# Optimization experiments

Measured on AMD Instinct MI355X. Metric: run time of the kernel, lower is better.

The kernel has to match this reference:

```python
import jax, jax.numpy as jnp
import numpy as np

N = 100000        # nodes
E = 1600000       # edges (avg degree 16)
F_IN = 128        # num_node_features
H = 64            # hidden_channels
F_EDGE = 8        # num_edge_features (output dim per edge)


def setup_inputs() -> dict:
    key = jax.random.key(0)
    ks = jax.random.split(key, 9)
    x = jax.random.normal(ks[0], (N, F_IN), dtype=jnp.float32)
    edge_index = jax.random.randint(ks[1], (2, E), 0, N, dtype=jnp.int32)
    s = 0.05
    W1 = jax.random.normal(ks[2], (F_IN, H), jnp.float32) * s
    b1 = jnp.zeros((H,), jnp.float32)
    W2 = jax.random.normal(ks[3], (H, H), jnp.float32) * s
    b2 = jnp.zeros((H,), jnp.float32)
    Wl = jax.random.normal(ks[4], (2 * H, F_EDGE), jnp.float32) * s
    bl = jnp.zeros((F_EDGE,), jnp.float32)
    return {"x": x, "edge_index": edge_index,
            "W1": W1, "b1": b1, "W2": W2, "b2": b2, "Wl": Wl, "bl": bl}


def gcn_conv(x, W, b, row, col, n):
    # GCNConv: h = D^{-1/2} (A + I) D^{-1/2} (x W) + b
    h = x @ W
    sl = jnp.arange(n, dtype=row.dtype)          # self-loops
    r = jnp.concatenate([row, sl])
    c = jnp.concatenate([col, sl])
    ones = jnp.ones(r.shape[0], dtype=h.dtype)
    deg = jax.ops.segment_sum(ones, c, num_segments=n)      # in-degree incl. self-loop
    dinv = jax.lax.rsqrt(jnp.maximum(deg, 1e-12))
    norm = dinv[r] * dinv[c]                                 # symmetric normalization
    agg = jax.ops.segment_sum(norm[:, None] * h[r], c, num_segments=n)
    return agg + b


def reference(x, edge_index, W1, b1, W2, b2, Wl, bl):
    row, col = edge_index[0], edge_index[1]
    h = jax.nn.relu(gcn_conv(x, W1, b1, row, col, N))
    # dropout p=0.5 is identity at inference (training=False)
    h = jax.nn.relu(gcn_conv(h, W2, b2, row, col, N))
    x_i = h[row]                                  # [E, H]
    x_j = h[col]                                  # [E, H]
    return jnp.concatenate([x_i, x_j], axis=-1) @ Wl + bl   # [E, F_EDGE]
```

## Files before the change

kernel.cpp:

```cpp
#include <hip/hip_runtime.h>
#include <hip/hip_bf16.h>

static constexpr int NN  = 100000;
static constexpr int NE  = 1600000;
static constexpr int FIN = 128;
static constexpr int HD  = 64;

static constexpr int NB    = 256;
static constexpr int NPB   = 392;
static constexpr int EPB   = NE / NB;
static constexpr unsigned long long DIV392_MAGIC = 43826197ULL;

typedef __attribute__((ext_vector_type(8))) short bf16x8;
typedef __attribute__((ext_vector_type(4))) float f32x4;

__device__ __forceinline__ float bf2f(unsigned short u) {
    return __uint_as_float(((unsigned int)u) << 16);
}
__device__ __forceinline__ unsigned short f2bf(float f) {
    __hip_bfloat16 hb = __float2bfloat16(f);
    return *(unsigned short*)&hb;
}
__device__ __forceinline__ int bucket_of(int c) {
    return (int)(((unsigned long long)(unsigned int)c * DIV392_MAGIC) >> 34);
}

__device__ __forceinline__ float load_in(const void* p, size_t i, int isbf) {
    return isbf ? bf2f(((const unsigned short*)p)[i]) : ((const float*)p)[i];
}

__global__ __launch_bounds__(256) void k_hist(const int* __restrict__ col, int* __restrict__ hist,
                                              const unsigned short* __restrict__ xu,
                                              int* __restrict__ flag) {
    __shared__ int h[4][NB];
    int t = threadIdx.x, w = t >> 6;
#pragma unroll
    for (int r = 0; r < 4; ++r) h[r][t] = 0;
    __syncthreads();
    int base = blockIdx.x * EPB;
    for (int e = base + t; e < base + EPB; e += 256)
        atomicAdd(&h[w][bucket_of(col[e])], 1);
    __syncthreads();
    hist[t * NB + blockIdx.x] = h[0][t] + h[1][t] + h[2][t] + h[3][t];
    if (blockIdx.x == 0) {
        __syncthreads();
        int cnt = 0;
        for (int k = t; k < 4096; k += 256) {
            unsigned short u = xu[2 * k];
            int ex = (u >> 7) & 0xFF;
            cnt += (ex >= 110 && ex <= 135) ? 1 : 0;
        }
        h[0][t] = cnt;
        __syncthreads();
        for (int off = 128; off > 0; off >>= 1) {
            if (t < off) h[0][t] += h[0][t + off];
            __syncthreads();
        }
        if (t == 0) flag[0] = (h[0][0] >= 2048) ? 1 : 0;
    }
}

__global__ __launch_bounds__(256) void k_gscan1(int* __restrict__ a, int* __restrict__ bsums) {
    __shared__ int sd[256];
    int t = threadIdx.x;
    int base = blockIdx.x * 1024 + t * 4;
    int v0 = a[base], v1 = a[base + 1], v2 = a[base + 2], v3 = a[base + 3];
    int tsum = v0 + v1 + v2 + v3;
    sd[t] = tsum;
    __syncthreads();
    for (int off = 1; off < 256; off <<= 1) {
        int tmp = (t >= off) ? sd[t - off] : 0;
        __syncthreads();
        sd[t] += tmp;
        __syncthreads();
    }
    int run = sd[t] - tsum;
    a[base] = run; run += v0;
    a[base + 1] = run; run += v1;
    a[base + 2] = run; run += v2;
    a[base + 3] = run;
    if (t == 255) bsums[blockIdx.x] = sd[t];
}

__device__ __forceinline__ void scan_bsums(const int* __restrict__ bsumsRaw, int* sb) {
    int t = threadIdx.x;
    int myv = 0;
    if (t < 64) { myv = bsumsRaw[t]; sb[t] = myv; }
    __syncthreads();
    for (int off = 1; off < 64; off <<= 1) {
        int v = (t < 64 && t >= off) ? sb[t - off] : 0;
        __syncthreads();
        if (t < 64) sb[t] += v;
        __syncthreads();
    }
    if (t < 64) sb[t] -= myv;
    __syncthreads();
}

__global__ __launch_bounds__(256) void k_binfill(const int* __restrict__ row, const int* __restrict__ col,
                                                 const int* __restrict__ histS,
                                                 const int* __restrict__ bsumsRaw,
                                                 int* __restrict__ csr_tmp) {
    __shared__ int cur[NB];
    __shared__ int sb[64];
    int t = threadIdx.x;
    scan_bsums(bsumsRaw, sb);
    cur[t] = histS[t * NB + blockIdx.x] + sb[t >> 2];
    __syncthreads();
    int base = blockIdx.x * EPB;
    for (int e = base + t; e < base + EPB; e += 256) {
        int r = row[e], c = col[e];
        int b = bucket_of(c);
        int p = atomicAdd(&cur[b], 1);
        csr_tmp[p] = r | ((c - b * NPB) << 17);
    }
}

__global__ __launch_bounds__(256) void k_bsort(const int* __restrict__ csr_tmp,
                                               const int* __restrict__ histS,
                                               const int* __restrict__ bsumsRaw,
                                               int* __restrict__ csr_src,
                                               int* __restrict__ start,
                                               float* __restrict__ dinv) {
    __shared__ int cnt[512];
    __shared__ int cur[512];
    __shared__ int sb[64];
    int t = threadIdx.x;
    int k = blockIdx.x;
    cnt[t] = 0; cnt[t + 256] = 0;
    scan_bsums(bsumsRaw, sb);
    int S = histS[k * NB] + sb[k >> 2];
    int E = (k < NB - 1) ? (histS[(k + 1) * NB] + sb[(k + 1) >> 2]) : NE;
    int nbase = k * NPB;
    __syncthreads();
    for (int e = S + t; e < E; e += 256)
        atomicAdd(&cnt[csr_tmp[e] >> 17], 1);
    __syncthreads();
    int rc0 = cnt[t], rc1 = cnt[t + 256];
    for (int d = 1; d < 512; d <<= 1) {
        int idx = (t + 1) * (d << 1) - 1;
        if (idx < 512) cnt[idx] += cnt[idx - d];
        __syncthreads();
    }
    if (t == 0) cnt[511] = 0;
    __syncthreads();
    for (int d = 256; d >= 1; d >>= 1) {
        int idx = (t + 1) * (d << 1) - 1;
        if (idx < 512) { int tmp = cnt[idx - d]; cnt[idx - d] = cnt[idx]; cnt[idx] += tmp; }
        __syncthreads();
    }
    int n0 = nbase + t;
    if (n0 < NN) {
        start[n0] = S + cnt[t] + rc0;
        dinv[n0] = rsqrtf((float)(rc0 + 1));
    }
    int li = t + 256;
    int n1 = nbase + li;
    if (li < NPB && n1 < NN) {
        start[n1] = S + cnt[li] + rc1;
        dinv[n1] = rsqrtf((float)(rc1 + 1));
    }
    cur[t] = cnt[t]; cur[t + 256] = cnt[t + 256];
    __syncthreads();
    for (int e = S + t; e < E; e += 256) {
        int u = csr_tmp[e];
        int p = atomicAdd(&cur[u >> 17], 1);
        csr_src[S + p] = u & 0x1FFFF;
    }
}

template <int K, bool XDUAL>
__global__ __launch_bounds__(256) void k_gemm_mfma(const void* __restrict__ X,
                                                   const void* __restrict__ W,
                                                   const float* __restrict__ dinv,
                                                   unsigned short* __restrict__ T,
                                                   const int* __restrict__ flag) {
    constexpr int KT = K / 32;
    __shared__ unsigned short Bs[KT * 4 * 64 * 8];
    int isbf = flag[0];
    for (int tup = threadIdx.x; tup < KT * 4 * 64; tup += 256) {
        int l  = tup & 63;
        int nt = (tup >> 6) & 3;
        int kt = tup >> 8;
        int n  = nt * 16 + (l & 15);
        int kb = kt * 32 + (l >> 4) * 8;
        unsigned short tmp[8];
#pragma unroll
        for (int j = 0; j < 8; ++j) tmp[j] = f2bf(load_in(W, (size_t)(kb + j) * HD + n, isbf));
        *((uint4*)&Bs[(size_t)tup * 8]) = *((const uint4*)tmp);
    }
    __syncthreads();
    int wave = threadIdx.x >> 6, lane = threadIdx.x & 63;
    int quad = lane >> 4, m = lane & 15;
    int row0 = blockIdx.x * 64 + wave * 16;
    int row  = row0 + m;
    int rowc = (row < NN) ? row : (NN - 1);
    bool xf32 = XDUAL && (isbf == 0);
    const char* xrow = (const char*)X + (size_t)rowc * K * (xf32 ? 4 : 2);
    f32x4 acc[4];
#pragma unroll
    for (int nt = 0; nt < 4; ++nt) acc[nt] = (f32x4){0.f, 0.f, 0.f, 0.f};
#pragma unroll
    for (int kt = 0; kt < KT; ++kt) {
        bf16x8 a;
        if (!xf32) {
            a = *((const bf16x8*)(xrow + (size_t)(kt * 32 + quad * 8) * 2));
        } else {
            const float4* fp = (const float4*)(xrow + (size_t)(kt * 32 + quad * 8) * 4);
            float4 u0 = fp[0], u1 = fp[1];
            unsigned short tmp[8] = {f2bf(u0.x), f2bf(u0.y), f2bf(u0.z), f2bf(u0.w),
                                     f2bf(u1.x), f2bf(u1.y), f2bf(u1.z), f2bf(u1.w)};
            a = *((const bf16x8*)tmp);
        }
#pragma unroll
        for (int nt = 0; nt < 4; ++nt) {
            bf16x8 b = *((const bf16x8*)&Bs[(size_t)((kt * 4 + nt) * 64 + lane) * 8]);
            acc[nt] = __builtin_amdgcn_mfma_f32_16x16x32_bf16(a, b, acc[nt], 0, 0, 0);
        }
    }
#pragma unroll
    for (int r = 0; r < 4; ++r) {
        int orow = row0 + quad * 4 + r;
        if (orow < NN) {
            float sc = dinv[orow];
#pragma unroll
            for (int nt = 0; nt < 4; ++nt)
                T[(size_t)orow * 64 + nt * 16 + m] = f2bf(acc[nt][r] * sc);
        }
    }
}

__device__ __forceinline__ void agg_to_lds(const unsigned short* __restrict__ T,
                                           const int* __restrict__ endOff,
                                           const int* __restrict__ csr_src,
                                           const float* __restrict__ dinv,
                                           const void* __restrict__ bias, int isbf,
                                           unsigned short (*hS)[72], int i0) {
    int lane = threadIdx.x & 63, wave = threadIdx.x >> 6;
    int g  = lane >> 3;
    int fl = (lane & 7) * 8;
    int li = wave * 8 + g;
    int i  = i0 + li;
    int end = endOff[i];
    int beg = (i == 0) ? 0 : endOff[i - 1];
    union U { uint4 u; unsigned short s[8]; };
    float a[8];
    {
        U t; t.u = *((const uint4*)(T + (size_t)i * 64 + fl));
#pragma unroll
        for (int j = 0; j < 8; ++j) a[j] = bf2f(t.s[j]);
    }
    int k = beg;
    for (; k + 3 < end; k += 4) {
        int s0 = csr_src[k], s1 = csr_src[k + 1], s2 = csr_src[k + 2], s3 = csr_src[k + 3];
        U t0, t1, t2, t3;
        t0.u = *((const uint4*)(T + (size_t)s0 * 64 + fl));
        t1.u = *((const uint4*)(T + (size_t)s1 * 64 + fl));
        t2.u = *((const uint4*)(T + (size_t)s2 * 64 + fl));
        t3.u = *((const uint4*)(T + (size_t)s3 * 64 + fl));
#pragma unroll
        for (int j = 0; j < 8; ++j)
            a[j] += bf2f(t0.s[j]) + bf2f(t1.s[j]) + bf2f(t2.s[j]) + bf2f(t3.s[j]);
    }
    for (; k < end; ++k) {
        int s = csr_src[k];
        U t; t.u = *((const uint4*)(T + (size_t)s * 64 + fl));
#pragma unroll
        for (int j = 0; j < 8; ++j) a[j] += bf2f(t.s[j]);
    }
    float di = dinv[i];
    U o;
#pragma unroll
    for (int j = 0; j < 8; ++j)
        o.s[j] = f2bf(fmaxf(fmaf(di, a[j], load_in(bias, fl + j, isbf)), 0.f));
    *((uint4*)&hS[li][fl]) = o.u;
}

__global__ __launch_bounds__(256) void k_agg_gemm(const unsigned short* __restrict__ T,
                                                  const int* __restrict__ endOff,
                                                  const int* __restrict__ csr_src,
                                                  const float* __restrict__ dinv,
                                                  const void* __restrict__ bias,
                                                  const void* __restrict__ W2,
                                                  const int* __restrict__ flag,
                                                  unsigned short* __restrict__ Tb) {
    __shared__ unsigned short hS[32][72];
    __shared__ unsigned short Bs[2 * 4 * 64 * 8];
    int isbf = flag[0];
    for (int tup = threadIdx.x; tup < 512; tup += 256) {
        int l  = tup & 63;
        int nt = (tup >> 6) & 3;
        int kt = tup >> 8;
        int n  = nt * 16 + (l & 15);
        int kb = kt * 32 + (l >> 4) * 8;
        unsigned short tmp[8];
#pragma unroll
        for (int j = 0; j < 8; ++j) tmp[j] = f2bf(load_in(W2, (size_t)(kb + j) * HD + n, isbf));
        *((uint4*)&Bs[(size_t)tup * 8]) = *((const uint4*)tmp);
    }
    int i0 = blockIdx.x * 32;
    agg_to_lds(T, endOff, csr_src, dinv, bias, isbf, hS, i0);
    __syncthreads();
    int wave = threadIdx.x >> 6, lane = threadIdx.x & 63;
    int quad = lane >> 4, m = lane & 15;
    int tile = wave >> 1;
    int nb   = (wave & 1) * 2;
    f32x4 acc0 = (f32x4){0.f, 0.f, 0.f, 0.f};
    f32x4 acc1 = (f32x4){0.f, 0.f, 0.f, 0.f};
#pragma unroll
    for (int kt = 0; kt < 2; ++kt) {
        bf16x8 a  = *((const bf16x8*)&hS[tile * 16 + m][kt * 32 + quad * 8]);
        bf16x8 b0 = *((const bf16x8*)&Bs[(size_t)((kt * 4 + nb) * 64 + lane) * 8]);
        bf16x8 b1 = *((const bf16x8*)&Bs[(size_t)((kt * 4 + nb + 1) * 64 + lane) * 8]);
        acc0 = __builtin_amdgcn_mfma_f32_16x16x32_bf16(a, b0, acc0, 0, 0, 0);
        acc1 = __builtin_amdgcn_mfma_f32_16x16x32_bf16(a, b1, acc1, 0, 0, 0);
    }
#pragma unroll
    for (int r = 0; r < 4; ++r) {
        int orow = i0 + tile * 16 + quad * 4 + r;
        float sc = dinv[orow];
        Tb[(size_t)orow * 64 + nb * 16 + m]       = f2bf(acc0[r] * sc);
        Tb[(size_t)orow * 64 + (nb + 1) * 16 + m] = f2bf(acc1[r] * sc);
    }
}

__global__ __launch_bounds__(256) void k_agg_pgemm(const unsigned short* __restrict__ T,
                                                   const int* __restrict__ endOff,
                                                   const int* __restrict__ csr_src,
                                                   const float* __restrict__ dinv,
                                                   const void* __restrict__ bias,
                                                   const void* __restrict__ Wl,
                                                   const void* __restrict__ bl,
                                                   const int* __restrict__ flag,
                                                   unsigned short* __restrict__ P) {
    __shared__ unsigned short hS[32][72];
    int isbf = flag[0];
    int lane = threadIdx.x & 63;
    int quad = lane >> 4, m = lane & 15;
    bf16x8 bfr[2];
#pragma unroll
    for (int kt = 0; kt < 2; ++kt) {
        unsigned short tmp[8];
#pragma unroll
        for (int j = 0; j < 8; ++j) {
            int kk = kt * 32 + quad * 8 + j;
            float w = (m < 8) ? load_in(Wl, (size_t)kk * 8 + m, isbf)
                              : load_in(Wl, (size_t)(64 + kk) * 8 + (m - 8), isbf);
            tmp[j] = f2bf(w);
        }
        bfr[kt] = *((const bf16x8*)tmp);
    }
    float binit = (m < 8) ? load_in(bl, m, isbf) : 0.f;
    int i0 = blockIdx.x * 32;
    agg_to_lds(T, endOff, csr_src, dinv, bias, isbf, hS, i0);
    __syncthreads();
    int wave = threadIdx.x >> 6;
    if (wave < 2) {
        f32x4 acc = (f32x4){binit, binit, binit, binit};
#pragma unroll
        for (int kt = 0; kt < 2; ++kt) {
            bf16x8 a = *((const bf16x8*)&hS[wave * 16 + m][kt * 32 + quad * 8]);
            acc = __builtin_amdgcn_mfma_f32_16x16x32_bf16(a, bfr[kt], acc, 0, 0, 0);
        }
#pragma unroll
        for (int r = 0; r < 4; ++r) {
            int orow = i0 + wave * 16 + quad * 4 + r;
            P[(size_t)orow * 16 + m] = f2bf(acc[r]);
        }
    }
}

__global__ __launch_bounds__(256) void k_edge_add(const unsigned short* __restrict__ P,
                                                  const int* __restrict__ erow,
                                                  const int* __restrict__ ecol,
                                                  void* __restrict__ out,
                                                  const int* __restrict__ flag) {
    int isbf = flag[0];
    int e = blockIdx.x * 256 + threadIdx.x;
    int i = erow[e], j = ecol[e];
    ushort4 r0 = *((const ushort4*)(P + (size_t)i * 16));
    ushort4 r1 = *((const ushort4*)(P + (size_t)i * 16 + 4));
    ushort4 c0 = *((const ushort4*)(P + (size_t)j * 16 + 8));
    ushort4 c1 = *((const ushort4*)(P + (size_t)j * 16 + 12));
    float v[8] = {bf2f(r0.x) + bf2f(c0.x), bf2f(r0.y) + bf2f(c0.y),
                  bf2f(r0.z) + bf2f(c0.z), bf2f(r0.w) + bf2f(c0.w),
                  bf2f(r1.x) + bf2f(c1.x), bf2f(r1.y) + bf2f(c1.y),
                  bf2f(r1.z) + bf2f(c1.z), bf2f(r1.w) + bf2f(c1.w)};
    if (isbf) {
        union { unsigned short h[8]; uint4 u; } p;
#pragma unroll
        for (int o = 0; o < 8; ++o) p.h[o] = f2bf(v[o]);
        *((uint4*)((__hip_bfloat16*)out + (size_t)e * 8)) = p.u;
    } else {
        float* op = (float*)out + (size_t)e * 8;
        ((float4*)op)[0] = make_float4(v[0], v[1], v[2], v[3]);
        ((float4*)op)[1] = make_float4(v[4], v[5], v[6], v[7]);
    }
}

extern "C" void kernel_launch(void* const* d_in, const int* in_sizes, int n_in,
                              void* d_out, int out_size, void* d_ws, size_t ws_size,
                              hipStream_t stream) {
    const void* x  = d_in[0];
    const int*  ei = (const int*)d_in[1];
    const void* W1 = d_in[2];
    const void* b1 = d_in[3];
    const void* W2 = d_in[4];
    const void* b2 = d_in[5];
    const void* Wl = d_in[6];
    const void* bl = d_in[7];
    const int* row = ei;
    const int* col = ei + NE;

    char* ws = (char*)d_ws;
    int*   flag    = (int*)ws;    ws += 16;
    int*   hist    = (int*)ws;    ws += (size_t)NB * NB * 4;
    int*   bsums   = (int*)ws;    ws += 256 * 4;
    int*   start   = (int*)ws;    ws += (size_t)NN * 4;
    float* dinv    = (float*)ws;  ws += (size_t)NN * 4;
    int*   csr_tmp = (int*)ws;    ws += (size_t)NE * 4;
    int*   csr_src = (int*)ws;    ws += (size_t)NE * 4;
    unsigned short* T  = (unsigned short*)ws;  ws += (size_t)NN * 64 * 2;
    unsigned short* Tb = (unsigned short*)ws;  ws += (size_t)NN * 64 * 2;
    unsigned short* P  = (unsigned short*)ws;

    int gE   = (NE + 255) / 256;
    int gN32 = NN / 32;
    int gN64 = (NN + 63) / 64;

    k_hist   <<<NB, 256, 0, stream>>>(col, hist, (const unsigned short*)x, flag);
    k_gscan1 <<<64, 256, 0, stream>>>(hist, bsums);
    k_binfill<<<NB, 256, 0, stream>>>(row, col, hist, bsums, csr_tmp);
    k_bsort  <<<NB, 256, 0, stream>>>(csr_tmp, hist, bsums, csr_src, start, dinv);

    k_gemm_mfma<FIN, true><<<gN64, 256, 0, stream>>>(x, W1, dinv, T, flag);

    k_agg_gemm <<<gN32, 256, 0, stream>>>(T, start, csr_src, dinv, b1, W2, flag, Tb);

    k_agg_pgemm<<<gN32, 256, 0, stream>>>(Tb, start, csr_src, dinv, b2, Wl, bl, flag, P);

    k_edge_add <<<gE, 256, 0, stream>>>(P, row, col, d_out, flag);
}
```

Before: 293.0 us.

## Split node features into 16-column slices and unfuse aggregation from GEMMs

Feature matrices are stored as four 16-column slices, each NN x 16 contiguous, so each aggregation block gathers from one 3.2MB slice that can stay cache-resident. Aggregation moves to a standalone kernel that splits each node's neighbour list across four lanes, combines their partial sums with shuffles, and adds the self term afterwards. The dense GEMMs become separate kernels that read the sliced layout. The cost is extra launches and a round trip through global memory for H4, in exchange for better cache locality and more parallelism in the gather.

```diff
diff --git a/kernel.cpp b/kernel.cpp
--- a/kernel.cpp
+++ b/kernel.cpp
@@ -10,6 +10,8 @@
 static constexpr int NPB   = 392;
 static constexpr int EPB   = NE / NB;
 static constexpr unsigned long long DIV392_MAGIC = 43826197ULL;
+
+static constexpr int NSL = 4;
 
 typedef __attribute__((ext_vector_type(8))) short bf16x8;
 typedef __attribute__((ext_vector_type(4))) float f32x4;
@@ -173,7 +175,7 @@
 __global__ __launch_bounds__(256) void k_gemm_mfma(const void* __restrict__ X,
                                                    const void* __restrict__ W,
                                                    const float* __restrict__ dinv,
-                                                   unsigned short* __restrict__ T,
+                                                   unsigned short* __restrict__ T4,
                                                    const int* __restrict__ flag) {
     constexpr int KT = K / 32;
     __shared__ unsigned short Bs[KT * 4 * 64 * 8];
@@ -225,66 +227,74 @@
             float sc = dinv[orow];
 #pragma unroll
             for (int nt = 0; nt < 4; ++nt)
-                T[(size_t)orow * 64 + nt * 16 + m] = f2bf(acc[nt][r] * sc);
-        }
-    }
-}
-
-__device__ __forceinline__ void agg_to_lds(const unsigned short* __restrict__ T,
-                                           const int* __restrict__ endOff,
-                                           const int* __restrict__ csr_src,
-                                           const float* __restrict__ dinv,
-                                           const void* __restrict__ bias, int isbf,
-                                           unsigned short (*hS)[72], int i0) {
-    int lane = threadIdx.x & 63, wave = threadIdx.x >> 6;
-    int g  = lane >> 3;
-    int fl = (lane & 7) * 8;
-    int li = wave * 8 + g;
-    int i  = i0 + li;
+                T4[((size_t)nt * NN + orow) * 16 + m] = f2bf(acc[nt][r] * sc);
+        }
+    }
+}
+
+__global__ __launch_bounds__(256) void k_agg4(const unsigned short* __restrict__ T4,
+                                              const int* __restrict__ endOff,
+                                              const int* __restrict__ csr_src,
+                                              const float* __restrict__ dinv,
+                                              const void* __restrict__ bias,
+                                              const int* __restrict__ flag,
+                                              unsigned short* __restrict__ H4) {
+    int isbf = flag[0];
+    int slice = blockIdx.x & 3;
+    int grp   = blockIdx.x >> 2;
+    int t = threadIdx.x;
+    int li   = t >> 3;
+    int slot = (t >> 1) & 3;
+    int fl   = (t & 1) * 8;
+    int i = grp * 32 + li;
     int end = endOff[i];
     int beg = (i == 0) ? 0 : endOff[i - 1];
+    const unsigned short* Ts = T4 + (size_t)slice * NN * 16;
     union U { uint4 u; unsigned short s[8]; };
     float a[8];
-    {
-        U t; t.u = *((const uint4*)(T + (size_t)i * 64 + fl));
-#pragma unroll
-        for (int j = 0; j < 8; ++j) a[j] = bf2f(t.s[j]);
-    }
-    int k = beg;
-    for (; k + 3 < end; k += 4) {
-        int s0 = csr_src[k], s1 = csr_src[k + 1], s2 = csr_src[k + 2], s3 = csr_src[k + 3];
-        U t0, t1, t2, t3;
-        t0.u = *((const uint4*)(T + (size_t)s0 * 64 + fl));
-        t1.u = *((const uint4*)(T + (size_t)s1 * 64 + fl));
-        t2.u = *((const uint4*)(T + (size_t)s2 * 64 + fl));
-        t3.u = *((const uint4*)(T + (size_t)s3 * 64 + fl));
-#pragma unroll
-        for (int j = 0; j < 8; ++j)
-            a[j] += bf2f(t0.s[j]) + bf2f(t1.s[j]) + bf2f(t2.s[j]) + bf2f(t3.s[j]);
-    }
-    for (; k < end; ++k) {
-        int s = csr_src[k];
-        U t; t.u = *((const uint4*)(T + (size_t)s * 64 + fl));
-#pragma unroll
-        for (int j = 0; j < 8; ++j) a[j] += bf2f(t.s[j]);
-    }
+#pragma unroll
+    for (int j = 0; j < 8; ++j) a[j] = 0.f;
+    int k = beg + slot;
+    int sA = (k < end) ? csr_src[k] : -1;
+    int sB = (k + 4 < end) ? csr_src[k + 4] : -1;
+    while (sA >= 0) {
+        U rA, rB;
+        rA.u = *((const uint4*)(Ts + (size_t)sA * 16 + fl));
+        bool hb = (sB >= 0);
+        if (hb) rB.u = *((const uint4*)(Ts + (size_t)sB * 16 + fl));
+        k += 8;
+        sA = (k < end) ? csr_src[k] : -1;
+        sB = (k + 4 < end) ? csr_src[k + 4] : -1;
+#pragma unroll
+        for (int j = 0; j < 8; ++j) a[j] += bf2f(rA.s[j]);
+        if (hb) {
+#pragma unroll
+            for (int j = 0; j < 8; ++j) a[j] += bf2f(rB.s[j]);
+        }
+    }
+#pragma unroll
+    for (int j = 0; j < 8; ++j) {
+        a[j] += __shfl_xor(a[j], 2, 64);
+        a[j] += __shfl_xor(a[j], 4, 64);
+    }
+    U sf; sf.u = *((const uint4*)(Ts + (size_t)i * 16 + fl));
     float di = dinv[i];
     U o;
 #pragma unroll
-    for (int j = 0; j < 8; ++j)
-        o.s[j] = f2bf(fmaxf(fmaf(di, a[j], load_in(bias, fl + j, isbf)), 0.f));
-    *((uint4*)&hS[li][fl]) = o.u;
-}
-
-__global__ __launch_bounds__(256) void k_agg_gemm(const unsigned short* __restrict__ T,
-                                                  const int* __restrict__ endOff,
-                                                  const int* __restrict__ csr_src,
-                                                  const float* __restrict__ dinv,
-                                                  const void* __restrict__ bias,
-                                                  const void* __restrict__ W2,
-                                                  const int* __restrict__ flag,
-                                                  unsigned short* __restrict__ Tb) {
-    __shared__ unsigned short hS[32][72];
+    for (int j = 0; j < 8; ++j) {
+        float v = a[j] + bf2f(sf.s[j]);
+        float b = load_in(bias, (size_t)(slice * 16 + fl + j), isbf);
+        o.s[j] = f2bf(fmaxf(fmaf(di, v, b), 0.f));
+    }
+    if (slot == 0)
+        *((uint4*)(H4 + ((size_t)slice * NN + i) * 16 + fl)) = o.u;
+}
+
+__global__ __launch_bounds__(256) void k_gemm_h(const unsigned short* __restrict__ H4,
+                                                const void* __restrict__ W,
+                                                const float* __restrict__ dinv,
+                                                unsigned short* __restrict__ Tb4,
+                                                const int* __restrict__ flag) {
     __shared__ unsigned short Bs[2 * 4 * 64 * 8];
     int isbf = flag[0];
     for (int tup = threadIdx.x; tup < 512; tup += 256) {
@@ -295,47 +305,47 @@
         int kb = kt * 32 + (l >> 4) * 8;
         unsigned short tmp[8];
 #pragma unroll
-        for (int j = 0; j < 8; ++j) tmp[j] = f2bf(load_in(W2, (size_t)(kb + j) * HD + n, isbf));
+        for (int j = 0; j < 8; ++j) tmp[j] = f2bf(load_in(W, (size_t)(kb + j) * HD + n, isbf));
         *((uint4*)&Bs[(size_t)tup * 8]) = *((const uint4*)tmp);
     }
-    int i0 = blockIdx.x * 32;
-    agg_to_lds(T, endOff, csr_src, dinv, bias, isbf, hS, i0);
     __syncthreads();
     int wave = threadIdx.x >> 6, lane = threadIdx.x & 63;
     int quad = lane >> 4, m = lane & 15;
-    int tile = wave >> 1;
-    int nb   = (wave & 1) * 2;
-    f32x4 acc0 = (f32x4){0.f, 0.f, 0.f, 0.f};
-    f32x4 acc1 = (f32x4){0.f, 0.f, 0.f, 0.f};
+    int row0 = blockIdx.x * 64 + wave * 16;
+    int row  = row0 + m;
+    int rowc = (row < NN) ? row : (NN - 1);
+    f32x4 acc[4];
+#pragma unroll
+    for (int nt = 0; nt < 4; ++nt) acc[nt] = (f32x4){0.f, 0.f, 0.f, 0.f};
 #pragma unroll
     for (int kt = 0; kt < 2; ++kt) {
-        bf16x8 a  = *((const bf16x8*)&hS[tile * 16 + m][kt * 32 + quad * 8]);
-        bf16x8 b0 = *((const bf16x8*)&Bs[(size_t)((kt * 4 + nb) * 64 + lane) * 8]);
-        bf16x8 b1 = *((const bf16x8*)&Bs[(size_t)((kt * 4 + nb + 1) * 64 + lane) * 8]);
-        acc0 = __builtin_amdgcn_mfma_f32_16x16x32_bf16(a, b0, acc0, 0, 0, 0);
-        acc1 = __builtin_amdgcn_mfma_f32_16x16x32_bf16(a, b1, acc1, 0, 0, 0);
+        int k0 = kt * 32 + quad * 8;
+        bf16x8 a = *((const bf16x8*)&H4[((size_t)(k0 >> 4) * NN + rowc) * 16 + (k0 & 15)]);
+#pragma unroll
+        for (int nt = 0; nt < 4; ++nt) {
+            bf16x8 b = *((const bf16x8*)&Bs[(size_t)((kt * 4 + nt) * 64 + lane) * 8]);
+            acc[nt] = __builtin_amdgcn_mfma_f32_16x16x32_bf16(a, b, acc[nt], 0, 0, 0);
+        }
     }
 #pragma unroll
     for (int r = 0; r < 4; ++r) {
-        int orow = i0 + tile * 16 + quad * 4 + r;
-        float sc = dinv[orow];
-        Tb[(size_t)orow * 64 + nb * 16 + m]       = f2bf(acc0[r] * sc);
-        Tb[(size_t)orow * 64 + (nb + 1) * 16 + m] = f2bf(acc1[r] * sc);
-    }
-}
-
-__global__ __launch_bounds__(256) void k_agg_pgemm(const unsigned short* __restrict__ T,
-                                                   const int* __restrict__ endOff,
-                                                   const int* __restrict__ csr_src,
-                                                   const float* __restrict__ dinv,
-                                                   const void* __restrict__ bias,
-                                                   const void* __restrict__ Wl,
-                                                   const void* __restrict__ bl,
-                                                   const int* __restrict__ flag,
-                                                   unsigned short* __restrict__ P) {
-    __shared__ unsigned short hS[32][72];
+        int orow = row0 + quad * 4 + r;
+        if (orow < NN) {
+            float sc = dinv[orow];
+#pragma unroll
+            for (int nt = 0; nt < 4; ++nt)
+                Tb4[((size_t)nt * NN + orow) * 16 + m] = f2bf(acc[nt][r] * sc);
+        }
+    }
+}
+
+__global__ __launch_bounds__(256) void k_pgemm_h(const unsigned short* __restrict__ H4,
+                                                 const void* __restrict__ Wl,
+                                                 const void* __restrict__ bl,
+                                                 unsigned short* __restrict__ P,
+                                                 const int* __restrict__ flag) {
     int isbf = flag[0];
-    int lane = threadIdx.x & 63;
+    int wave = threadIdx.x >> 6, lane = threadIdx.x & 63;
     int quad = lane >> 4, m = lane & 15;
     bf16x8 bfr[2];
 #pragma unroll
@@ -351,22 +361,20 @@
         bfr[kt] = *((const bf16x8*)tmp);
     }
     float binit = (m < 8) ? load_in(bl, m, isbf) : 0.f;
-    int i0 = blockIdx.x * 32;
-    agg_to_lds(T, endOff, csr_src, dinv, bias, isbf, hS, i0);
-    __syncthreads();
-    int wave = threadIdx.x >> 6;
-    if (wave < 2) {
-        f32x4 acc = (f32x4){binit, binit, binit, binit};
-#pragma unroll
-        for (int kt = 0; kt < 2; ++kt) {
-            bf16x8 a = *((const bf16x8*)&hS[wave * 16 + m][kt * 32 + quad * 8]);
-            acc = __builtin_amdgcn_mfma_f32_16x16x32_bf16(a, bfr[kt], acc, 0, 0, 0);
-        }
-#pragma unroll
-        for (int r = 0; r < 4; ++r) {
-            int orow = i0 + wave * 16 + quad * 4 + r;
-            P[(size_t)orow * 16 + m] = f2bf(acc[r]);
-        }
+    int row0 = blockIdx.x * 64 + wave * 16;
+    int row  = row0 + m;
+    int rowc = (row < NN) ? row : (NN - 1);
+    f32x4 acc = (f32x4){binit, binit, binit, binit};
+#pragma unroll
+    for (int kt = 0; kt < 2; ++kt) {
+        int k0 = kt * 32 + quad * 8;
+        bf16x8 a = *((const bf16x8*)&H4[((size_t)(k0 >> 4) * NN + rowc) * 16 + (k0 & 15)]);
+        acc = __builtin_amdgcn_mfma_f32_16x16x32_bf16(a, bfr[kt], acc, 0, 0, 0);
+    }
+#pragma unroll
+    for (int r = 0; r < 4; ++r) {
+        int orow = row0 + quad * 4 + r;
+        if (orow < NN) P[(size_t)orow * 16 + m] = f2bf(acc[r]);
     }
 }
 
@@ -420,24 +428,26 @@
     float* dinv    = (float*)ws;  ws += (size_t)NN * 4;
     int*   csr_tmp = (int*)ws;    ws += (size_t)NE * 4;
     int*   csr_src = (int*)ws;    ws += (size_t)NE * 4;
-    unsigned short* T  = (unsigned short*)ws;  ws += (size_t)NN * 64 * 2;
-    unsigned short* Tb = (unsigned short*)ws;  ws += (size_t)NN * 64 * 2;
-    unsigned short* P  = (unsigned short*)ws;
+    unsigned short* T4  = (unsigned short*)ws;  ws += (size_t)NN * 64 * 2;
+    unsigned short* H4  = (unsigned short*)ws;  ws += (size_t)NN * 64 * 2;
+    unsigned short* Tb4 = (unsigned short*)ws;  ws += (size_t)NN * 64 * 2;
+    unsigned short* P   = (unsigned short*)ws;
 
     int gE   = (NE + 255) / 256;
-    int gN32 = NN / 32;
     int gN64 = (NN + 63) / 64;
+    int gAgg = (NN / 32) * NSL;
 
     k_hist   <<<NB, 256, 0, stream>>>(col, hist, (const unsigned short*)x, flag);
     k_gscan1 <<<64, 256, 0, stream>>>(hist, bsums);
     k_binfill<<<NB, 256, 0, stream>>>(row, col, hist, bsums, csr_tmp);
     k_bsort  <<<NB, 256, 0, stream>>>(csr_tmp, hist, bsums, csr_src, start, dinv);
 
-    k_gemm_mfma<FIN, true><<<gN64, 256, 0, stream>>>(x, W1, dinv, T, flag);
-
-    k_agg_gemm <<<gN32, 256, 0, stream>>>(T, start, csr_src, dinv, b1, W2, flag, Tb);
-
-    k_agg_pgemm<<<gN32, 256, 0, stream>>>(Tb, start, csr_src, dinv, b2, Wl, bl, flag, P);
-
-    k_edge_add <<<gE, 256, 0, stream>>>(P, row, col, d_out, flag);
-}
+    k_gemm_mfma<FIN, true><<<gN64, 256, 0, stream>>>(x, W1, dinv, T4, flag);
+    k_agg4 <<<gAgg, 256, 0, stream>>>(T4, start, csr_src, dinv, b1, flag, H4);
+
+    k_gemm_h<<<gN64, 256, 0, stream>>>(H4, W2, dinv, Tb4, flag);
+    k_agg4 <<<gAgg, 256, 0, stream>>>(Tb4, start, csr_src, dinv, b2, flag, H4);
+
+    k_pgemm_h<<<gN64, 256, 0, stream>>>(H4, Wl, bl, P, flag);
+    k_edge_add<<<gE, 256, 0, stream>>>(P, row, col, d_out, flag);
+}
```

Measured after the change: 299.5 us. 1.02x slower.
